# Performance work log

Hardware: AMD Instinct MI355X
Metric: run time of the kernel (lower is better)

## Reference

```python
import jax, jax.numpy as jnp
import numpy as np

B, K, U, P, H, L = 4096, 512, 3, 5, 128, 32
N_SUB = 10
RATE_LO, RATE_HI = 0.01, 3.0


def setup_inputs() -> dict:
    key = jax.random.key(0)
    ks = jax.random.split(key, 8)
    f32 = jnp.float32
    return {
        "y0": jax.random.uniform(ks[0], (B, P), dtype=f32),
        "u_seq": jax.random.uniform(ks[1], (B, K, U), dtype=f32),
        "dt_seq": jax.random.uniform(ks[2], (B, K), dtype=f32),
        "lift_W": jax.random.normal(ks[3], (L, U + P), dtype=f32) * 0.1,
        "lift_b": jnp.zeros((L,), f32),
        "W_ih": jax.random.normal(ks[4], (3 * H, L), dtype=f32) * 0.1,
        "W_hh": jax.random.normal(ks[5], (3 * H, H), dtype=f32) * 0.1,
        "b_ih": jnp.zeros((3 * H,), f32),
        "b_hh": jnp.zeros((3 * H,), f32),
        "head_W": jax.random.normal(ks[6], (8, H), dtype=f32) * 0.1,
        "head_b": jnp.zeros((8,), f32),
        "u_to_x_jump": jax.random.uniform(ks[7], (U, P), dtype=f32) * 0.1,
    }


def _rhs(y, theta):
    # y: (B,5) [A,D,G,J,M], theta: (B,8) [kf1..kf4, kr1..kr4]
    A, D, G, J, M = (y[..., i] for i in range(5))
    kf1, kf2, kf3, kf4, kr1, kr2, kr3, kr4 = (theta[..., i] for i in range(8))
    dA = -kf1 * A + kr1 * D
    dD = kf1 * A - kr1 * D - kf2 * D + kr2 * G
    dG = kf2 * D - kr2 * G - kf3 * G + kr3 * J
    dJ = kf3 * G - kr3 * J - kf4 * J + kr4 * M
    dM = kf4 * J - kr4 * M
    return jnp.stack([dA, dD, dG, dJ, dM], axis=-1)


def _rk4_step(y, dt, theta):
    # y: (B,5), dt: (B,1), theta: (B,8)
    k1 = _rhs(y, theta)
    k2 = _rhs(y + 0.5 * dt * k1, theta)
    k3 = _rhs(y + 0.5 * dt * k2, theta)
    k4 = _rhs(y + dt * k3, theta)
    y_next = y + dt / 6.0 * (k1 + 2.0 * k2 + 2.0 * k3 + k4)
    return jnp.maximum(y_next, 0.0)  # clamp_min(0)


def reference(y0, u_seq, dt_seq, lift_W, lift_b, W_ih, W_hh, b_ih, b_hh,
              head_W, head_b, u_to_x_jump):
    Bd = y0.shape[0]

    def step(carry, xs):
        y_prev, h = carry
        u_k, dt_k = xs  # (B,U), (B,)
        # lift on [u_k, detached y_prev]
        feat = jnp.concatenate([u_k, jax.lax.stop_gradient(y_prev)], axis=-1)
        x = jax.nn.silu(feat @ lift_W.T + lift_b)
        # single-layer GRU cell (torch gate order: r, z, n)
        gi = x @ W_ih.T + b_ih    # (B,3H)
        gh = h @ W_hh.T + b_hh    # (B,3H)
        r = jax.nn.sigmoid(gi[:, :H] + gh[:, :H])
        z = jax.nn.sigmoid(gi[:, H:2 * H] + gh[:, H:2 * H])
        n = jnp.tanh(gi[:, 2 * H:] + r * gh[:, 2 * H:])
        h_new = (1.0 - z) * n + z * h
        raw = h_new @ head_W.T + head_b
        theta = RATE_LO + (RATE_HI - RATE_LO) * jax.nn.sigmoid(raw)
        # input-induced state jump, then RK4 with N_SUB substeps
        y = y_prev + u_k @ u_to_x_jump
        hsub = (dt_k / float(N_SUB))[:, None]
        for _ in range(N_SUB):  # small fixed substep count
            y = _rk4_step(y, hsub, theta)
        return (y, h_new), (y, theta)

    y_prev0 = y0 + 0.01
    h0 = jnp.zeros((Bd, H), y0.dtype)
    xs = (jnp.swapaxes(u_seq, 0, 1), dt_seq.T)  # (K,B,U), (K,B)
    _, (y_out, theta_out) = jax.lax.scan(step, (y_prev0, h0), xs)
    y_out = jnp.swapaxes(y_out, 0, 1)          # (B,K,5)
    theta_out = jnp.swapaxes(theta_out, 0, 1)  # (B,K,8)
    return y_out, theta_out
```

## Files before the change

### kernel.cpp

```cpp
#include <hip/hip_runtime.h>


#define KSTEPS 512
#define NTH 512

typedef short s16x8 __attribute__((ext_vector_type(8)));
typedef short s16x4 __attribute__((ext_vector_type(4)));
typedef float f32x4 __attribute__((ext_vector_type(4)));
typedef float f32x2 __attribute__((ext_vector_type(2)));

__device__ __forceinline__ unsigned short f2bf(float f) {
  union { float f; unsigned u; } v; v.f = f;
  unsigned r = v.u + 0x7FFFu + ((v.u >> 16) & 1u);
  return (unsigned short)(r >> 16);
}
__device__ __forceinline__ unsigned cvt2bf(float lo, float hi) {
  unsigned r;
  asm("v_cvt_pk_bf16_f32 %0, %1, %2" : "=v"(r) : "v"(lo), "v"(hi));
  return r;
}
__device__ __forceinline__ float ex2(float x) {
#if __has_builtin(__builtin_amdgcn_exp2f)
  return __builtin_amdgcn_exp2f(x);
#else
  return exp2f(x);
#endif
}
__device__ __forceinline__ float rcp_(float x) {
#if __has_builtin(__builtin_amdgcn_rcpf)
  return __builtin_amdgcn_rcpf(x);
#else
  return 1.0f / x;
#endif
}
__device__ __forceinline__ float sigm(float x) {
  return rcp_(1.0f + ex2(-1.44269504088896f * x));
}
__device__ __forceinline__ float tanh_(float x) {
  return fmaf(2.0f, rcp_(1.0f + ex2(-2.88539008177793f * x)), -1.0f);
}
__device__ __forceinline__ f32x4 splat4(float v) { f32x4 r = {v, v, v, v}; return r; }
__device__ __forceinline__ f32x4 MFMA(s16x8 a, s16x8 b, f32x4 c) {
  return __builtin_amdgcn_mfma_f32_16x16x32_bf16(a, b, c, 0, 0, 0);
}
__device__ __forceinline__ s16x8 bfrag_g(const float* __restrict__ src8) {
  s16x8 r;
#pragma unroll
  for (int j = 0; j < 8; ++j) r[j] = (short)f2bf(src8[j]);
  return r;
}

__device__ __forceinline__ f32x2 pkfma_blo(f32x2 a, f32x2 b, f32x2 c) {
  f32x2 d;
  asm("v_pk_fma_f32 %0, %1, %2, %3 op_sel:[0,0,0] op_sel_hi:[1,0,1]"
      : "=v"(d) : "v"(a), "v"(b), "v"(c));
  return d;
}
__device__ __forceinline__ f32x2 pkfma_bhi(f32x2 a, f32x2 b, f32x2 c) {
  f32x2 d;
  asm("v_pk_fma_f32 %0, %1, %2, %3 op_sel:[0,1,0] op_sel_hi:[1,1,1]"
      : "=v"(d) : "v"(a), "v"(b), "v"(c));
  return d;
}
__device__ __forceinline__ f32x2 pkmul_blo(f32x2 a, f32x2 b) {
  f32x2 d;
  asm("v_pk_mul_f32 %0, %1, %2 op_sel:[0,0] op_sel_hi:[1,0]"
      : "=v"(d) : "v"(a), "v"(b));
  return d;
}
__device__ __forceinline__ f32x2 pkmul_bhi(f32x2 a, f32x2 b) {
  f32x2 d;
  asm("v_pk_mul_f32 %0, %1, %2 op_sel:[0,1] op_sel_hi:[1,1]"
      : "=v"(d) : "v"(a), "v"(b));
  return d;
}
__device__ __forceinline__ f32x2 pkadd(f32x2 a, f32x2 b) {
  f32x2 d;
  asm("v_pk_add_f32 %0, %1, %2" : "=v"(d) : "v"(a), "v"(b));
  return d;
}

__global__ __launch_bounds__(NTH, 2) void rnn_scan_kernel(
    const float* __restrict__ y0, const float* __restrict__ u_seq,
    const float* __restrict__ dt_seq, const float* __restrict__ lift_W,
    const float* __restrict__ lift_b, const float* __restrict__ W_ih,
    const float* __restrict__ W_hh, const float* __restrict__ b_ih,
    const float* __restrict__ b_hh, const float* __restrict__ head_W,
    const float* __restrict__ head_b, const float* __restrict__ jumpW,
    float* __restrict__ y_out, float* __restrict__ th_out) {
  __shared__ __align__(16) unsigned short s_Ah[4096];
  __shared__ __align__(16) unsigned short s_Ax[1024];
  __shared__ __align__(16) float s_thr[2][16][8];
  __shared__ __align__(16) float s_yr[2][16][8];
  __shared__ __align__(16) float s_ur[3][16][4];

  const int tid = threadIdx.x;
  const int w = tid >> 6;
  const int lane = tid & 63;
  const int quad = lane >> 4;
  const int col = lane & 15;
  const int r0 = blockIdx.x << 4;

  s16x8 zf;
#pragma unroll
  for (int j = 0; j < 8; ++j) zf[j] = 0;

  s16x8 bih_r = bfrag_g(&W_ih[(w * 16 + col) * 32 + quad * 8]);
  s16x8 bih_z = bfrag_g(&W_ih[((8 + w) * 16 + col) * 32 + quad * 8]);
  s16x8 bih_n = bfrag_g(&W_ih[((16 + w) * 16 + col) * 32 + quad * 8]);
  s16x8 bhh_r[4], bhh_z[4], bhh_n[4], bhdF[4], bhdR[4];
#pragma unroll
  for (int s = 0; s < 4; ++s) {
    bhh_r[s] = bfrag_g(&W_hh[(w * 16 + col) * 128 + s * 32 + quad * 8]);
    bhh_z[s] = bfrag_g(&W_hh[((8 + w) * 16 + col) * 128 + s * 32 + quad * 8]);
    bhh_n[s] = bfrag_g(&W_hh[((16 + w) * 16 + col) * 128 + s * 32 + quad * 8]);
    bhdF[s] = bfrag_g(&head_W[(col & 3) * 128 + s * 32 + quad * 8]);
    bhdR[s] = bfrag_g(&head_W[(4 + (col & 3)) * 128 + s * 32 + quad * 8]);
  }
  s16x8 blft0 = (quad == 0) ? bfrag_g(&lift_W[col * 8]) : zf;
  s16x8 blft1 = (quad == 0) ? bfrag_g(&lift_W[(16 + col) * 8]) : zf;

  f32x4 brz_r, brz_z, bn_iv, bn_hv, lbv0, lbv1, hbF, hbR;
#pragma unroll
  for (int i = 0; i < 4; ++i) {
    int g = w * 16 + quad * 4 + i;
    brz_r[i] = b_ih[g] + b_hh[g];
    brz_z[i] = b_ih[128 + g] + b_hh[128 + g];
    bn_iv[i] = b_ih[256 + g];
    bn_hv[i] = b_hh[256 + g];
    lbv0[i] = lift_b[quad * 4 + i];
    lbv1[i] = lift_b[16 + quad * 4 + i];
    hbF[i] = head_b[i];
    hbR[i] = head_b[4 + i];
  }
  float J[15];
#pragma unroll
  for (int i = 0; i < 15; ++i) J[i] = jumpW[i];

  const int hwoff = (((w >> 1) * 64 + ((w & 1) * 2 + (quad >> 1)) * 16 + col) << 4) +
                    ((quad & 1) << 3);
  const int xw0 = ((((quad >> 1)) * 16 + col) << 4) + ((quad & 1) << 3);
  const int xw1 = (((2 + (quad >> 1)) * 16 + col) << 4) + ((quad & 1) << 3);

  f32x4 ar = brz_r, az = brz_z, angi = bn_iv, angh = bn_hv;
  f32x4 h_reg = splat4(0.0f);
  float y[5] = {0.f, 0.f, 0.f, 0.f, 0.f};

  if (w == 1 && lane < 16) {
#pragma unroll
    for (int pk = 0; pk < 2; ++pk) {
      const float* up = &u_seq[((size_t)(r0 + lane) * KSTEPS + pk) * 3];
      f32x4 uv;
      uv[0] = up[0]; uv[1] = up[1]; uv[2] = up[2];
      uv[3] = dt_seq[(size_t)(r0 + lane) * KSTEPS + pk];
      *(f32x4*)&s_ur[pk][lane][0] = uv;
    }
  }
  if (w == 7) {
    float uc0 = 0.f, uc1 = 0.f, uc2 = 0.f;
    if (quad == 0) {
      const float* yp = &y0[(r0 + col) * 5];
#pragma unroll
      for (int i = 0; i < 5; ++i) y[i] = yp[i] + 0.01f;
      const float* up = &u_seq[((size_t)(r0 + col) * KSTEPS) * 3];
      uc0 = up[0]; uc1 = up[1]; uc2 = up[2];
    }
    s16x8 af = zf;
    if (quad == 0) {
      union { s16x8 v; unsigned u[4]; } afu;
      afu.u[0] = cvt2bf(uc0, uc1);
      afu.u[1] = cvt2bf(uc2, y[0]);
      afu.u[2] = cvt2bf(y[1], y[2]);
      afu.u[3] = cvt2bf(y[3], y[4]);
      af = afu.v;
    }
    f32x4 x0 = MFMA(blft0, af, lbv0);
    f32x4 x1 = MFMA(blft1, af, lbv1);
    f32x4 s0, s1;
#pragma unroll
    for (int i = 0; i < 4; ++i) {
      float v0 = x0[i]; s0[i] = v0 * sigm(v0);
      float v1 = x1[i]; s1[i] = v1 * sigm(v1);
    }
    uint2 xp0, xp1;
    xp0.x = cvt2bf(s0[0], s0[1]); xp0.y = cvt2bf(s0[2], s0[3]);
    xp1.x = cvt2bf(s1[0], s1[1]); xp1.y = cvt2bf(s1[2], s1[3]);
    *(uint2*)((char*)s_Ax + xw0) = xp0;
    *(uint2*)((char*)s_Ax + xw1) = xp1;
  }
  __syncthreads();

  int sA = 0, sB = 1, sC = 2;

#pragma unroll 1
  for (int k = 0; k < KSTEPS; ++k) {
    {
      s16x8 xf = *(const s16x8*)((const char*)s_Ax + lane * 16);
      ar = MFMA(bih_r, xf, ar);
      az = MFMA(bih_z, xf, az);
      angi = MFMA(bih_n, xf, bn_iv);
    }
    {
      f32x4 hf;
#pragma unroll
      for (int i = 0; i < 4; ++i) {
        float r = sigm(ar[i]);
        float z = sigm(az[i]);
        float n = tanh_(fmaf(r, angh[i], angi[i]));
        float hn = fmaf(z, h_reg[i] - n, n);
        h_reg[i] = hn;
        hf[i] = hn;
      }
      uint2 hp;
      hp.x = cvt2bf(hf[0], hf[1]);
      hp.y = cvt2bf(hf[2], hf[3]);
      *(uint2*)((char*)s_Ah + hwoff) = hp;
    }
    __syncthreads();

    s16x8 ah[4];
#pragma unroll
    for (int s = 0; s < 4; ++s)
      ah[s] = *(const s16x8*)((const char*)s_Ah + (s * 64 + lane) * 16);

    if (w == 7) {
      __builtin_amdgcn_s_setprio(1);
      f32x4 urk = *(const f32x4*)&s_ur[sA][col][0];
      f32x4 urk1 = *(const f32x4*)&s_ur[sB][col][0];
      f32x4 hdF0 = MFMA(bhdF[0], ah[0], hbF);
      f32x4 hdF1 = MFMA(bhdF[1], ah[1], splat4(0.0f));
      f32x4 hdF2 = MFMA(bhdF[2], ah[2], splat4(0.0f));
      f32x4 hdF3 = MFMA(bhdF[3], ah[3], splat4(0.0f));
      f32x4 hdR0 = MFMA(bhdR[0], ah[0], hbR);
      f32x4 hdR1 = MFMA(bhdR[1], ah[1], splat4(0.0f));
      f32x4 hdR2 = MFMA(bhdR[2], ah[2], splat4(0.0f));
      f32x4 hdR3 = MFMA(bhdR[3], ah[3], splat4(0.0f));
      ar = MFMA(bhh_r[0], ah[0], brz_r);
      az = MFMA(bhh_z[0], ah[0], brz_z);
      angh = MFMA(bhh_n[0], ah[0], bn_hv);
#pragma unroll
      for (int s = 1; s < 4; ++s) {
        ar = MFMA(bhh_r[s], ah[s], ar);
        az = MFMA(bhh_z[s], ah[s], az);
        angh = MFMA(bhh_n[s], ah[s], angh);
      }
      f32x4 hdF = (hdF0 + hdF1) + (hdF2 + hdF3);
      f32x4 hdR = (hdR0 + hdR1) + (hdR2 + hdR3);
      f32x4 tvF, tvR;
#pragma unroll
      for (int i = 0; i < 4; ++i) {
        tvF[i] = fmaf(2.99f, sigm(hdF[i]), 0.01f);
        tvR[i] = fmaf(2.99f, sigm(hdR[i]), 0.01f);
      }
      const int slot = k & 1;
      if (quad == 0) {
        *(f32x4*)&s_thr[slot][col][0] = tvF;
        *(f32x4*)&s_thr[slot][col][4] = tvR;
      }
      const float F0 = tvF[0], F1 = tvF[1], F2 = tvF[2], F3 = tvF[3];
      const float R0 = tvR[0], R1 = tvR[1], R2 = tvR[2], R3 = tvR[3];
#pragma unroll
      for (int i = 0; i < 5; ++i)
        y[i] += urk[0] * J[i] + urk[1] * J[5 + i] + urk[2] * J[10 + i];
      const float hs = urk[3] * 0.1f;

      const float TD0 = -(F0 + R0), TD1 = -(F1 + R1), TD2 = -(F2 + R2), TD3 = -(F3 + R3);
      const float c4 = 0.25f * hs, c3 = hs * (1.0f / 3.0f), c2 = 0.5f * hs;
      const float d30 = fmaf(c4, TD0, 1.f), d31 = fmaf(c4, TD1, 1.f);
      const float d32 = fmaf(c4, TD2, 1.f), d33 = fmaf(c4, TD3, 1.f);
      const float l31 = c4 * F1, l32 = c4 * F2, l33 = c4 * F3;
      const float u30 = c4 * R0, u31 = c4 * R1, u32 = c4 * R2;
      const float w300 = fmaf(TD0, d30, R0 * l31);
      const float w301 = fmaf(TD0, u30, R0 * d31);
      const float w302 = R0 * u31;
      const float w310 = fmaf(F1, d30, TD1 * l31);
      const float w311 = fmaf(F1, u30, fmaf(TD1, d31, R1 * l32));
      const float w312 = fmaf(TD1, u31, R1 * d32);
      const float w313 = R1 * u32;
      const float w320 = F2 * l31;
      const float w321 = fmaf(F2, d31, TD2 * l32);
      const float w322 = fmaf(F2, u31, fmaf(TD2, d32, R2 * l33));
      const float w323 = fmaf(TD2, u32, R2 * d33);
      const float w331 = F3 * l32;
      const float w332 = fmaf(F3, d32, TD3 * l33);
      const float w333 = fmaf(F3, u32, TD3 * d33);
      const float e20 = fmaf(c3, w300, 1.f), e21 = fmaf(c3, w311, 1.f);
      const float e22 = fmaf(c3, w322, 1.f), e23 = fmaf(c3, w333, 1.f);
      const float a201 = c3 * w301, a202 = c3 * w302;
      const float a210 = c3 * w310, a212 = c3 * w312, a213 = c3 * w313;
      const float a220 = c3 * w320, a221 = c3 * w321, a223 = c3 * w323;
      const float a231 = c3 * w331, a232 = c3 * w332;
      const float w200 = fmaf(TD0, e20, R0 * a210);
      const float w201 = fmaf(TD0, a201, R0 * e21);
      const float w202 = fmaf(TD0, a202, R0 * a212);
      const float w203 = R0 * a213;
      const float w210 = fmaf(F1, e20, fmaf(TD1, a210, R1 * a220));
      const float w211 = fmaf(F1, a201, fmaf(TD1, e21, R1 * a221));
      const float w212 = fmaf(F1, a202, fmaf(TD1, a212, R1 * e22));
      const float w213 = fmaf(TD1, a213, R1 * a223);
      const float w220 = fmaf(F2, a210, TD2 * a220);
      const float w221 = fmaf(F2, e21, fmaf(TD2, a221, R2 * a231));
      const float w222 = fmaf(F2, a212, fmaf(TD2, e22, R2 * a232));
      const float w223 = fmaf(F2, a213, fmaf(TD2, a223, R2 * e23));
      const float w230 = F3 * a220;
      const float w231 = fmaf(F3, a221, TD3 * a231);
      const float w232 = fmaf(F3, e22, TD3 * a232);
      const float w233 = fmaf(F3, a223, TD3 * e23);
      const float z100 = fmaf(c2, w200, 1.f), z101 = c2 * w201, z102 = c2 * w202, z103 = c2 * w203;
      const float z110 = c2 * w210, z111 = fmaf(c2, w211, 1.f), z112 = c2 * w212, z113 = c2 * w213;
      const float z120 = c2 * w220, z121 = c2 * w221, z122 = fmaf(c2, w222, 1.f), z123 = c2 * w223;
      const float z130 = c2 * w230, z131 = c2 * w231, z132 = c2 * w232, z133 = fmaf(c2, w233, 1.f);

      f32x2 cZa0 = {z100, z110}, cZb0 = {z120, z130};
      f32x2 cZa1 = {z101, z111}, cZb1 = {z121, z131};
      f32x2 cZa2 = {z102, z112}, cZb2 = {z122, z132};
      f32x2 cZa3 = {z103, z113}, cZb3 = {z123, z133};

      const float FH0 = hs * F0, FH1 = hs * F1, FH2 = hs * F2, FH3 = hs * F3;
      const float RH0 = hs * R0, RH1 = hs * R1, RH2 = hs * R2, RH3 = hs * R3;
      const float TDH0 = -(FH0 + RH0), TDH1 = -(FH1 + RH1);
      const float TDH2 = -(FH2 + RH2), TDH3 = -(FH3 + RH3);
      f32x2 pA01 = {TDH0, FH1}, pB01 = {RH0, TDH1}, pC01 = {0.f, RH1};
      f32x2 pA23 = {FH2, 0.f}, pB23 = {TDH2, FH3}, pC23 = {RH2, TDH3};
      f32x2 cG0a = pkfma_blo(pC01, cZb0, pkfma_bhi(pB01, cZa0, pkmul_blo(pA01, cZa0)));
      f32x2 cG1a = pkfma_blo(pC01, cZb1, pkfma_bhi(pB01, cZa1, pkmul_blo(pA01, cZa1)));
      f32x2 cG2a = pkfma_blo(pC01, cZb2, pkfma_bhi(pB01, cZa2, pkmul_blo(pA01, cZa2)));
      f32x2 cG3a = pkfma_blo(pC01, cZb3, pkfma_bhi(pB01, cZa3, pkmul_blo(pA01, cZa3)));
      f32x2 cG0b = pkfma_bhi(pC23, cZb0, pkfma_blo(pB23, cZb0, pkmul_bhi(pA23, cZa0)));
      f32x2 cG1b = pkfma_bhi(pC23, cZb1, pkfma_blo(pB23, cZb1, pkmul_bhi(pA23, cZa1)));
      f32x2 cG2b = pkfma_bhi(pC23, cZb2, pkfma_blo(pB23, cZb2, pkmul_bhi(pA23, cZa2)));
      f32x2 cG3b = pkfma_bhi(pC23, cZb3, pkfma_blo(pB23, cZb3, pkmul_bhi(pA23, cZa3)));
      cG0a[0] += 1.0f;
      cG1a[1] += 1.0f;
      cG2b[0] += 1.0f;
      cG3b[1] += 1.0f;

      const float w0v = fmaf(FH0, y[0], -(RH0 * y[1]));
      const float w1v = fmaf(FH1, y[1], -(RH1 * y[2]));
      const float w2v = fmaf(FH2, y[2], -(RH2 * y[3]));
      const float w3v = fmaf(FH3, y[3], -(RH3 * y[4]));
      f32x2 W01 = {w0v, w1v}, W23 = {w2v, w3v};
      f32x2 A01 = W01, A23 = W23;
#pragma unroll
      for (int ss = 0; ss < 9; ++ss) {
        f32x2 m01 = pkfma_blo(cG0a, W01,
                    pkfma_bhi(cG1a, W01,
                    pkfma_blo(cG2a, W23, pkmul_bhi(cG3a, W23))));
        f32x2 m23 = pkfma_blo(cG0b, W01,
                    pkfma_bhi(cG1b, W01,
                    pkfma_blo(cG2b, W23, pkmul_bhi(cG3b, W23))));
        W01 = m01; W23 = m23;
        A01 = pkadd(A01, m01); A23 = pkadd(A23, m23);
      }
      f32x2 s01 = pkfma_blo(cZa0, A01,
                  pkfma_bhi(cZa1, A01,
                  pkfma_blo(cZa2, A23, pkmul_bhi(cZa3, A23))));
      f32x2 s23 = pkfma_blo(cZb0, A01,
                  pkfma_bhi(cZb1, A01,
                  pkfma_blo(cZb2, A23, pkmul_bhi(cZb3, A23))));
      const float s0f = s01[0], s1f = s01[1], s2f = s23[0], s3f = s23[1];
      y[0] -= s0f;
      y[1] += s0f - s1f;
      y[2] += s1f - s2f;
      y[3] += s2f - s3f;
      y[4] += s3f;
      if (quad == 0) {
        *(f32x4*)&s_yr[slot][col][0] = *(const f32x4*)&y[0];
        s_yr[slot][col][4] = y[4];
      }
      if (k + 1 < KSTEPS) {
        s16x8 af = zf;
        if (quad == 0) {
          union { s16x8 v; unsigned u[4]; } afu;
          afu.u[0] = cvt2bf(urk1[0], urk1[1]);
          afu.u[1] = cvt2bf(urk1[2], y[0]);
          afu.u[2] = cvt2bf(y[1], y[2]);
          afu.u[3] = cvt2bf(y[3], y[4]);
          af = afu.v;
        }
        f32x4 x0 = MFMA(blft0, af, lbv0);
        f32x4 x1 = MFMA(blft1, af, lbv1);
        f32x4 s0, s1;
#pragma unroll
        for (int i = 0; i < 4; ++i) {
          float v0 = x0[i]; s0[i] = v0 * sigm(v0);
          float v1 = x1[i]; s1[i] = v1 * sigm(v1);
        }
        uint2 xp0, xp1;
        xp0.x = cvt2bf(s0[0], s0[1]); xp0.y = cvt2bf(s0[2], s0[3]);
        xp1.x = cvt2bf(s1[0], s1[1]); xp1.y = cvt2bf(s1[2], s1[3]);
        *(uint2*)((char*)s_Ax + xw0) = xp0;
        *(uint2*)((char*)s_Ax + xw1) = xp1;
      }
      __builtin_amdgcn_s_setprio(0);
    } else {
      ar = MFMA(bhh_r[0], ah[0], brz_r);
      az = MFMA(bhh_z[0], ah[0], brz_z);
      angh = MFMA(bhh_n[0], ah[0], bn_hv);
#pragma unroll
      for (int s = 1; s < 4; ++s) {
        ar = MFMA(bhh_r[s], ah[s], ar);
        az = MFMA(bhh_z[s], ah[s], az);
        angh = MFMA(bhh_n[s], ah[s], angh);
      }
      if (w == 1 && lane < 16) {
        int kn2 = (k + 2 < KSTEPS) ? k + 2 : KSTEPS - 1;
        const float* up = &u_seq[((size_t)(r0 + lane) * KSTEPS + kn2) * 3];
        f32x4 uv;
        uv[0] = up[0]; uv[1] = up[1]; uv[2] = up[2];
        uv[3] = dt_seq[(size_t)(r0 + lane) * KSTEPS + kn2];
        *(f32x4*)&s_ur[sC][lane][0] = uv;
      }
      if (w == 0 && k > 0) {
        const int km = k - 1, slot = km & 1;
#pragma unroll
        for (int rep = 0; rep < 2; ++rep) {
          int idx = lane + rep * 64;
          int row = idx >> 3, c = idx & 7;
          th_out[((size_t)(r0 + row) * KSTEPS + km) * 8 + c] = s_thr[slot][row][c];
        }
        {
          int idx = lane;
          int row = idx / 5, c = idx - row * 5;
          y_out[((size_t)(r0 + row) * KSTEPS + km) * 5 + c] = s_yr[slot][row][c];
        }
        if (lane < 16) {
          int idx = 64 + lane;
          int row = idx / 5, c = idx - row * 5;
          y_out[((size_t)(r0 + row) * KSTEPS + km) * 5 + c] = s_yr[slot][row][c];
        }
      }
    }
    __syncthreads();
    int st = sA; sA = sB; sB = sC; sC = st;
  }

  if (w == 0) {
    const int km = KSTEPS - 1, slot = km & 1;
#pragma unroll
    for (int rep = 0; rep < 2; ++rep) {
      int idx = lane + rep * 64;
      int row = idx >> 3, c = idx & 7;
      th_out[((size_t)(r0 + row) * KSTEPS + km) * 8 + c] = s_thr[slot][row][c];
    }
    {
      int idx = lane;
      int row = idx / 5, c = idx - row * 5;
      y_out[((size_t)(r0 + row) * KSTEPS + km) * 5 + c] = s_yr[slot][row][c];
    }
    if (lane < 16) {
      int idx = 64 + lane;
      int row = idx / 5, c = idx - row * 5;
      y_out[((size_t)(r0 + row) * KSTEPS + km) * 5 + c] = s_yr[slot][row][c];
    }
  }
}

extern "C" void kernel_launch(void* const* d_in, const int* in_sizes, int n_in,
                              void* d_out, int out_size, void* d_ws, size_t ws_size,
                              hipStream_t stream) {
  const float* y0 = (const float*)d_in[0];
  const float* u_seq = (const float*)d_in[1];
  const float* dt_seq = (const float*)d_in[2];
  const float* lift_W = (const float*)d_in[3];
  const float* lift_b = (const float*)d_in[4];
  const float* W_ih = (const float*)d_in[5];
  const float* W_hh = (const float*)d_in[6];
  const float* b_ih = (const float*)d_in[7];
  const float* b_hh = (const float*)d_in[8];
  const float* head_W = (const float*)d_in[9];
  const float* head_b = (const float*)d_in[10];
  const float* jumpW = (const float*)d_in[11];

  float* y_out = (float*)d_out;
  float* th_out = y_out + (size_t)4096 * 512 * 5;

  rnn_scan_kernel<<<dim3(256), dim3(NTH), 0, stream>>>(
      y0, u_seq, dt_seq, lift_W, lift_b, W_ih, W_hh, b_ih, b_hh, head_W,
      head_b, jumpW, y_out, th_out);
}
```

Before: 960.0 us.

## Halve rows per block to launch 512 blocks and fill all CUs

Each block now handles 8 batch rows instead of 16 and the grid doubles to 512 blocks. The launch bound rises to 4 blocks per CU. With 256 blocks on a GPU that has more compute units than that, many CUs sat idle during the serial 512-step scan; more blocks spreads the sequential latency-bound work across the whole device. In exchange, half of each 16-wide MFMA tile is wasted on duplicated rows, and the tighter register budget from the new launch bound may cause spills.

```diff
diff --git a/kernel.cpp b/kernel.cpp
--- a/kernel.cpp
+++ b/kernel.cpp
@@ -3,6 +3,7 @@
 
 #define KSTEPS 512
 #define NTH 512
+#define NROWS 8
 
 typedef short s16x8 __attribute__((ext_vector_type(8)));
 typedef short s16x4 __attribute__((ext_vector_type(4)));
@@ -80,7 +81,7 @@
   return d;
 }
 
-__global__ __launch_bounds__(NTH, 2) void rnn_scan_kernel(
+__global__ __launch_bounds__(NTH, 4) void rnn_scan_kernel(
     const float* __restrict__ y0, const float* __restrict__ u_seq,
     const float* __restrict__ dt_seq, const float* __restrict__ lift_W,
     const float* __restrict__ lift_b, const float* __restrict__ W_ih,
@@ -92,14 +93,15 @@
   __shared__ __align__(16) unsigned short s_Ax[1024];
   __shared__ __align__(16) float s_thr[2][16][8];
   __shared__ __align__(16) float s_yr[2][16][8];
-  __shared__ __align__(16) float s_ur[3][16][4];
+  __shared__ __align__(16) float s_ur[3][8][4];
 
   const int tid = threadIdx.x;
   const int w = tid >> 6;
   const int lane = tid & 63;
   const int quad = lane >> 4;
   const int col = lane & 15;
-  const int r0 = blockIdx.x << 4;
+  const int rc = col & 7;
+  const int r0 = blockIdx.x << 3;
 
   s16x8 zf;
 #pragma unroll
@@ -146,7 +148,7 @@
   f32x4 h_reg = splat4(0.0f);
   float y[5] = {0.f, 0.f, 0.f, 0.f, 0.f};
 
-  if (w == 1 && lane < 16) {
+  if (w == 1 && lane < NROWS) {
 #pragma unroll
     for (int pk = 0; pk < 2; ++pk) {
       const float* up = &u_seq[((size_t)(r0 + lane) * KSTEPS + pk) * 3];
@@ -159,10 +161,10 @@
   if (w == 7) {
     float uc0 = 0.f, uc1 = 0.f, uc2 = 0.f;
     if (quad == 0) {
-      const float* yp = &y0[(r0 + col) * 5];
+      const float* yp = &y0[(r0 + rc) * 5];
 #pragma unroll
       for (int i = 0; i < 5; ++i) y[i] = yp[i] + 0.01f;
-      const float* up = &u_seq[((size_t)(r0 + col) * KSTEPS) * 3];
+      const float* up = &u_seq[((size_t)(r0 + rc) * KSTEPS) * 3];
       uc0 = up[0]; uc1 = up[1]; uc2 = up[2];
     }
     s16x8 af = zf;
@@ -225,8 +227,8 @@
 
     if (w == 7) {
       __builtin_amdgcn_s_setprio(1);
-      f32x4 urk = *(const f32x4*)&s_ur[sA][col][0];
-      f32x4 urk1 = *(const f32x4*)&s_ur[sB][col][0];
+      f32x4 urk = *(const f32x4*)&s_ur[sA][rc][0];
+      f32x4 urk1 = *(const f32x4*)&s_ur[sB][rc][0];
       f32x4 hdF0 = MFMA(bhdF[0], ah[0], hbF);
       f32x4 hdF1 = MFMA(bhdF[1], ah[1], splat4(0.0f));
       f32x4 hdF2 = MFMA(bhdF[2], ah[2], splat4(0.0f));
@@ -403,7 +405,7 @@
         az = MFMA(bhh_z[s], ah[s], az);
         angh = MFMA(bhh_n[s], ah[s], angh);
       }
-      if (w == 1 && lane < 16) {
+      if (w == 1 && lane < NROWS) {
         int kn2 = (k + 2 < KSTEPS) ? k + 2 : KSTEPS - 1;
         const float* up = &u_seq[((size_t)(r0 + lane) * KSTEPS + kn2) * 3];
         f32x4 uv;
@@ -413,22 +415,14 @@
       }
       if (w == 0 && k > 0) {
         const int km = k - 1, slot = km & 1;
-#pragma unroll
-        for (int rep = 0; rep < 2; ++rep) {
-          int idx = lane + rep * 64;
-          int row = idx >> 3, c = idx & 7;
+        {
+          int row = lane >> 3, c = lane & 7;
           th_out[((size_t)(r0 + row) * KSTEPS + km) * 8 + c] = s_thr[slot][row][c];
         }
-        {
-          int idx = lane;
-          int row = idx / 5, c = idx - row * 5;
+        if (lane < 40) {
+          int row = lane / 5, c = lane - row * 5;
           y_out[((size_t)(r0 + row) * KSTEPS + km) * 5 + c] = s_yr[slot][row][c];
         }
-        if (lane < 16) {
-          int idx = 64 + lane;
-          int row = idx / 5, c = idx - row * 5;
-          y_out[((size_t)(r0 + row) * KSTEPS + km) * 5 + c] = s_yr[slot][row][c];
-        }
       }
     }
     __syncthreads();
@@ -437,20 +431,12 @@
 
   if (w == 0) {
     const int km = KSTEPS - 1, slot = km & 1;
-#pragma unroll
-    for (int rep = 0; rep < 2; ++rep) {
-      int idx = lane + rep * 64;
-      int row = idx >> 3, c = idx & 7;
+    {
+      int row = lane >> 3, c = lane & 7;
       th_out[((size_t)(r0 + row) * KSTEPS + km) * 8 + c] = s_thr[slot][row][c];
     }
-    {
-      int idx = lane;
-      int row = idx / 5, c = idx - row * 5;
-      y_out[((size_t)(r0 + row) * KSTEPS + km) * 5 + c] = s_yr[slot][row][c];
-    }
-    if (lane < 16) {
-      int idx = 64 + lane;
-      int row = idx / 5, c = idx - row * 5;
+    if (lane < 40) {
+      int row = lane / 5, c = lane - row * 5;
       y_out[((size_t)(r0 + row) * KSTEPS + km) * 5 + c] = s_yr[slot][row][c];
     }
   }
@@ -475,7 +461,7 @@
   float* y_out = (float*)d_out;
   float* th_out = y_out + (size_t)4096 * 512 * 5;
 
-  rnn_scan_kernel<<<dim3(256), dim3(NTH), 0, stream>>>(
+  rnn_scan_kernel<<<dim3(512), dim3(NTH), 0, stream>>>(
       y0, u_seq, dt_seq, lift_W, lift_b, W_ih, W_hh, b_ih, b_hh, head_W,
       head_b, jumpW, y_out, th_out);
 }
```

After: 3.771 ms. 3.93x slower.
